# Kernel tuning notes

Hardware: AMD Instinct MI355X
Metric: run time of the kernel (lower is better)

## Reference

```python
import jax, jax.numpy as jnp
import numpy as np

N_HEAD = 16

def setup_inputs() -> dict:
    key = jax.random.key(0)
    k1, k2, k3, k4, k5 = jax.random.split(key, 5)
    B, T, C = 4, 2048, 1024
    s = 0.02
    x = jax.random.normal(k1, (B, T, C), dtype=jnp.float32)
    W_attn = jax.random.normal(k2, (C, 3 * C), dtype=jnp.float32) * s
    b_attn = jnp.zeros((3 * C,), dtype=jnp.float32)
    W_proj = jax.random.normal(k3, (C, C), dtype=jnp.float32) * s
    b_proj = jnp.zeros((C,), dtype=jnp.float32)
    return {"x": x, "W_attn": W_attn, "b_attn": b_attn, "W_proj": W_proj, "b_proj": b_proj}

def reference(x, W_attn, b_attn, W_proj, b_proj):
    B, T, C = x.shape
    H = N_HEAD
    hd = C // H
    qkv = x @ W_attn + b_attn                       # [B,T,3C]
    q, k, v = jnp.split(qkv, 3, axis=-1)            # each [B,T,C]
    # [B,H,T,hd]
    q = q.reshape(B, T, H, hd).transpose(0, 2, 1, 3)
    k = k.reshape(B, T, H, hd).transpose(0, 2, 1, 3)
    v = v.reshape(B, T, H, hd).transpose(0, 2, 1, 3)
    att = jnp.einsum('bhqd,bhkd->bhqk', q, k) * (1.0 / jnp.sqrt(jnp.float32(hd)))
    causal = jnp.tril(jnp.ones((T, T), dtype=bool))
    att = jnp.where(causal[None, None], att, jnp.float32(-jnp.inf))
    att = jax.nn.softmax(att, axis=-1)
    y = jnp.einsum('bhqk,bhkd->bhqd', att, v)       # [B,H,T,hd]
    y = y.transpose(0, 2, 1, 3).reshape(B, T, C)
    return y @ W_proj + b_proj
```

## Files before the change

### kernel.cpp

```cpp
#include <hip/hip_runtime.h>
#include <hip/hip_bf16.h>

typedef __bf16 bf16x8 __attribute__((ext_vector_type(8)));
typedef float f32x4 __attribute__((ext_vector_type(4)));

static __device__ __forceinline__ unsigned short f32_to_bf16(float f) {
    union { float f; unsigned u; } v; v.f = f;
    unsigned u = v.u;
    u += 0x7FFFu + ((u >> 16) & 1u);
    return (unsigned short)(u >> 16);
}
static __device__ __forceinline__ unsigned pack_bf16x2(float a, float b) {
    return ((unsigned)f32_to_bf16(a)) | (((unsigned)f32_to_bf16(b)) << 16);
}

static __device__ __forceinline__ void async_load16(const unsigned short* g,
                                                    unsigned short* l) {
    __builtin_amdgcn_global_load_lds(
        (__attribute__((address_space(1))) const unsigned int*)(const void*)g,
        (__attribute__((address_space(3))) unsigned int*)(void*)l,
        16, 0, 0);
}

__global__ void cast_f32_bf16(const float* __restrict__ src,
                              unsigned short* __restrict__ dst, int n4) {
    int i = blockIdx.x * blockDim.x + threadIdx.x;
    if (i < n4) {
        float4 f = ((const float4*)src)[i];
        ushort4 o;
        o.x = f32_to_bf16(f.x); o.y = f32_to_bf16(f.y);
        o.z = f32_to_bf16(f.z); o.w = f32_to_bf16(f.w);
        ((ushort4*)dst)[i] = o;
    }
}

__global__ void transpose_cast(const float* __restrict__ src,
                               unsigned short* __restrict__ dst, int R, int C) {
    __shared__ float tile[32][33];
    int c0 = blockIdx.x * 32, r0 = blockIdx.y * 32;
    int tx = threadIdx.x, ty = threadIdx.y;
    #pragma unroll
    for (int i = 0; i < 32; i += 8)
        tile[ty + i][tx] = src[(long)(r0 + ty + i) * C + c0 + tx];
    __syncthreads();
    #pragma unroll
    for (int i = 0; i < 32; i += 8)
        dst[(long)(c0 + ty + i) * R + r0 + tx] = f32_to_bf16(tile[tx][ty + i]);
}

template<bool OUT_BF16>
__global__ __launch_bounds__(256) void gemm_bt_bias(
    const unsigned short* __restrict__ A,
    const unsigned short* __restrict__ Bt,
    const float* __restrict__ bias,
    void* __restrict__ Cout,
    int M, int N, int K, int scale_ncols, float scale)
{
    __shared__ __align__(16) unsigned short As[128 * 64];
    __shared__ __align__(16) unsigned short Bs[128 * 64];

    const int tid  = threadIdx.x;
    const int m0   = blockIdx.x * 128;
    const int n0   = blockIdx.y * 128;
    const int w    = tid >> 6, lane = tid & 63;
    const int quad = lane >> 4, lr = lane & 15;
    const int wm   = (w >> 1) * 64, wn = (w & 1) * 64;

    f32x4 acc[4][4];
    #pragma unroll
    for (int i = 0; i < 4; i++)
        #pragma unroll
        for (int j = 0; j < 4; j++)
            acc[i][j] = (f32x4){0.f, 0.f, 0.f, 0.f};

    const int srow8 = lane >> 3;
    const int skoff = (lane & 7) * 8;

    for (int k0 = 0; k0 < K; k0 += 64) {
        __syncthreads();
        #pragma unroll
        for (int c = 0; c < 4; c++) {
            const int rbase = c * 32 + w * 8;
            async_load16(&A [(long)(m0 + rbase + srow8) * K + k0 + skoff], &As[rbase * 64]);
            async_load16(&Bt[(long)(n0 + rbase + srow8) * K + k0 + skoff], &Bs[rbase * 64]);
        }
        __syncthreads();

        #pragma unroll
        for (int ks = 0; ks < 2; ks++) {
            bf16x8 af[4], bfr[4];
            #pragma unroll
            for (int i = 0; i < 4; i++)
                af[i] = *(const bf16x8*)&As[(wm + i * 16 + lr) * 64 + ks * 32 + quad * 8];
            #pragma unroll
            for (int j = 0; j < 4; j++)
                bfr[j] = *(const bf16x8*)&Bs[(wn + j * 16 + lr) * 64 + ks * 32 + quad * 8];
            #pragma unroll
            for (int i = 0; i < 4; i++)
                #pragma unroll
                for (int j = 0; j < 4; j++)
                    acc[i][j] = __builtin_amdgcn_mfma_f32_16x16x32_bf16(af[i], bfr[j], acc[i][j], 0, 0, 0);
        }
    }

    #pragma unroll
    for (int i = 0; i < 4; i++) {
        #pragma unroll
        for (int j = 0; j < 4; j++) {
            int gcol = n0 + wn + j * 16 + lr;
            float bv = bias[gcol];
            float sc = (gcol < scale_ncols) ? scale : 1.0f;
            #pragma unroll
            for (int r = 0; r < 4; r++) {
                int grow = m0 + wm + i * 16 + quad * 4 + r;
                float v = (acc[i][j][r] + bv) * sc;
                if (OUT_BF16)
                    ((unsigned short*)Cout)[(long)grow * N + gcol] = f32_to_bf16(v);
                else
                    ((float*)Cout)[(long)grow * N + gcol] = v;
            }
        }
    }
}

__global__ __launch_bounds__(256) void transpose_v(
    const unsigned short* __restrict__ qkv,
    unsigned short* __restrict__ vT,
    int T, int C3, int C, int H)
{
    __shared__ __align__(16) unsigned short tile[64 * 72];
    const int tid = threadIdx.x;
    const int t0 = blockIdx.x * 64, h = blockIdx.y, b = blockIdx.z;
    const long ibase = ((long)b * T + t0) * C3 + 2 * C + h * 64;
    #pragma unroll
    for (int c = tid; c < 512; c += 256) {
        int r = c >> 3, off = (c & 7) * 8;
        *(uint4*)&tile[r * 72 + off] = *(const uint4*)&qkv[ibase + (long)r * C3 + off];
    }
    __syncthreads();
    const long obase = (long)((b * H + h) * 64) * T + t0;
    #pragma unroll
    for (int c = tid; c < 512; c += 256) {
        int d = c & 63, tc = c >> 6;
        unsigned short tmp[8];
        #pragma unroll
        for (int j = 0; j < 8; j++)
            tmp[j] = tile[(tc * 8 + j) * 72 + d];
        *(uint4*)&vT[obase + (long)d * T + tc * 8] = *(const uint4*)tmp;
    }
}

__global__ __launch_bounds__(256, 3) void attn_mfma(
    const unsigned short* __restrict__ qkv,
    const unsigned short* __restrict__ vT,
    unsigned short* __restrict__ yb,
    int T, int C3, int C, int H, int NT)
{
    constexpr int SQ = 72;
    __shared__ __align__(16) unsigned short Ks[64 * SQ];
    __shared__ __align__(16) unsigned short Vs[64 * SQ];
    __shared__ __align__(16) unsigned short Ps[128 * SQ];

    const int tid = threadIdx.x;
    const int h   = blockIdx.y;
    const int b   = blockIdx.z;
    const long rowbase = (long)b * T;
    const long vtbase  = (long)((b * H + h) * 64) * T;

    const int w = tid >> 6, lane = tid & 63;
    const int quad = lane >> 4, lr = lane & 15;

    const int r0 = tid >> 3, off0 = (tid & 7) * 8;
    const int r1 = r0 + 32;

    for (int t = 0; t < 2; t++) {
        const int qt = (t == 0) ? blockIdx.x : (NT - 1 - blockIdx.x);
        const int q0 = qt * 128;
        const int nb = 2 * qt + 2;

        const int wrow0 = w * 32;
        const int wrowmax = q0 + wrow0 + 31;

        bf16x8 aq[2][2];
        #pragma unroll
        for (int st = 0; st < 2; st++)
            #pragma unroll
            for (int ks = 0; ks < 2; ks++)
                aq[st][ks] = *(const bf16x8*)&qkv[
                    (rowbase + q0 + wrow0 + st * 16 + lr) * (long)C3 + h * 64 + ks * 32 + quad * 8];

        uint4 pk0, pk1, pv0, pv1;
        {
            long g0 = (rowbase + r0) * (long)C3 + C + h * 64 + off0;
            long g1 = (rowbase + r1) * (long)C3 + C + h * 64 + off0;
            pk0 = *(const uint4*)&qkv[g0];
            pk1 = *(const uint4*)&qkv[g1];
            pv0 = *(const uint4*)&vT[vtbase + (long)r0 * T + off0];
            pv1 = *(const uint4*)&vT[vtbase + (long)r1 * T + off0];
        }

        f32x4 oA[2][4];
        float lp[2] = {0.f, 0.f};
        #pragma unroll
        for (int st = 0; st < 2; st++)
            #pragma unroll
            for (int j = 0; j < 4; j++) oA[st][j] = (f32x4){0.f, 0.f, 0.f, 0.f};

        for (int kb = 0; kb < nb; kb++) {
            __syncthreads();
            *(uint4*)&Ks[r0 * SQ + off0] = pk0;
            *(uint4*)&Ks[r1 * SQ + off0] = pk1;
            *(uint4*)&Vs[r0 * SQ + off0] = pv0;
            *(uint4*)&Vs[r1 * SQ + off0] = pv1;
            __syncthreads();

            if (kb + 1 < nb) {
                long g0 = (rowbase + (kb + 1) * 64 + r0) * (long)C3 + C + h * 64 + off0;
                long g1 = (rowbase + (kb + 1) * 64 + r1) * (long)C3 + C + h * 64 + off0;
                pk0 = *(const uint4*)&qkv[g0];
                pk1 = *(const uint4*)&qkv[g1];
                pv0 = *(const uint4*)&vT[vtbase + (long)r0 * T + (kb + 1) * 64 + off0];
                pv1 = *(const uint4*)&vT[vtbase + (long)r1 * T + (kb + 1) * 64 + off0];
            }

            if (kb * 64 > wrowmax) continue;

            f32x4 sT[2][4];
            #pragma unroll
            for (int st = 0; st < 2; st++)
                #pragma unroll
                for (int j = 0; j < 4; j++) sT[st][j] = (f32x4){0.f, 0.f, 0.f, 0.f};
            #pragma unroll
            for (int ks = 0; ks < 2; ks++) {
                #pragma unroll
                for (int jt = 0; jt < 4; jt++) {
                    bf16x8 kf = *(const bf16x8*)&Ks[(jt * 16 + lr) * SQ + ks * 32 + quad * 8];
                    sT[0][jt] = __builtin_amdgcn_mfma_f32_16x16x32_bf16(kf, aq[0][ks], sT[0][jt], 0, 0, 0);
                    sT[1][jt] = __builtin_amdgcn_mfma_f32_16x16x32_bf16(kf, aq[1][ks], sT[1][jt], 0, 0, 0);
                }
            }

            const bool diag = (kb * 64 + 63 > q0 + wrow0);
            #pragma unroll
            for (int st = 0; st < 2; st++) {
                const int qg = q0 + wrow0 + st * 16 + lr;
                float rowsum = 0.f;
                #pragma unroll
                for (int jt = 0; jt < 4; jt++) {
                    float p[4];
                    #pragma unroll
                    for (int r = 0; r < 4; r++) {
                        float sv = sT[st][jt][r];
                        if (diag && (kb * 64 + jt * 16 + quad * 4 + r) > qg) sv = -1e30f;
                        p[r] = __builtin_amdgcn_exp2f(sv);
                        rowsum += p[r];
                    }
                    *(uint2*)&Ps[(wrow0 + st * 16 + lr) * SQ + jt * 16 + quad * 4] =
                        make_uint2(pack_bf16x2(p[0], p[1]), pack_bf16x2(p[2], p[3]));
                }
                lp[st] += rowsum;
            }

            #pragma unroll
            for (int ks = 0; ks < 2; ks++) {
                bf16x8 ap0 = *(const bf16x8*)&Ps[(wrow0 + lr) * SQ + ks * 32 + quad * 8];
                bf16x8 ap1 = *(const bf16x8*)&Ps[(wrow0 + 16 + lr) * SQ + ks * 32 + quad * 8];
                #pragma unroll
                for (int jt = 0; jt < 4; jt++) {
                    bf16x8 bv = *(const bf16x8*)&Vs[(jt * 16 + lr) * SQ + ks * 32 + quad * 8];
                    oA[0][jt] = __builtin_amdgcn_mfma_f32_16x16x32_bf16(ap0, bv, oA[0][jt], 0, 0, 0);
                    oA[1][jt] = __builtin_amdgcn_mfma_f32_16x16x32_bf16(ap1, bv, oA[1][jt], 0, 0, 0);
                }
            }
        }

        #pragma unroll
        for (int st = 0; st < 2; st++) {
            float l = lp[st];
            l += __shfl_xor(l, 16);
            l += __shfl_xor(l, 32);
            float inv = 1.f / l;
            #pragma unroll
            for (int r = 0; r < 4; r++) {
                float invr = __shfl(inv, quad * 4 + r, 16);
                long grow = rowbase + q0 + wrow0 + st * 16 + quad * 4 + r;
                #pragma unroll
                for (int jt = 0; jt < 4; jt++)
                    yb[grow * C + h * 64 + jt * 16 + lr] = f32_to_bf16(oA[st][jt][r] * invr);
            }
        }
    }
}

extern "C" void kernel_launch(void* const* d_in, const int* in_sizes, int n_in,
                              void* d_out, int out_size, void* d_ws, size_t ws_size,
                              hipStream_t stream) {
    const float* x      = (const float*)d_in[0];
    const float* W_attn = (const float*)d_in[1];
    const float* b_attn = (const float*)d_in[2];
    const float* W_proj = (const float*)d_in[3];
    const float* b_proj = (const float*)d_in[4];
    float* out = (float*)d_out;

    const int B = 4, T = 2048, C = 1024, H = 16;
    const int M  = B * T;
    const int C3 = 3 * C;
    const int NT = T / 128;
    const float scale2 = 0.18033688011112042f;

    char* ws = (char*)d_ws;
    size_t off = 0;
    auto carve = [&](size_t bytes) {
        char* p = ws + off;
        off += (bytes + 255) & ~(size_t)255;
        return p;
    };
    unsigned short* xb   = (unsigned short*)carve((size_t)M * C * 2);
    unsigned short* wat  = (unsigned short*)carve((size_t)C3 * C * 2);
    unsigned short* wpt  = (unsigned short*)carve((size_t)C * C * 2);
    unsigned short* qkvb = (unsigned short*)carve((size_t)M * C3 * 2);
    unsigned short* ybuf = (unsigned short*)carve((size_t)M * C * 2);
    unsigned short* vTb  = xb;

    cast_f32_bf16<<<(M * C / 4 + 255) / 256, 256, 0, stream>>>(x, xb, M * C / 4);
    transpose_cast<<<dim3(C3 / 32, C / 32), dim3(32, 8), 0, stream>>>(W_attn, wat, C, C3);
    transpose_cast<<<dim3(C / 32, C / 32), dim3(32, 8), 0, stream>>>(W_proj, wpt, C, C);

    gemm_bt_bias<true><<<dim3(M / 128, C3 / 128), 256, 0, stream>>>(
        xb, wat, b_attn, qkvb, M, C3, C, C, scale2);

    transpose_v<<<dim3(T / 64, H, B), 256, 0, stream>>>(qkvb, vTb, T, C3, C, H);

    attn_mfma<<<dim3(NT / 2, H, B), 256, 0, stream>>>(qkvb, vTb, ybuf, T, C3, C, H, NT);

    gemm_bt_bias<false><<<dim3(M / 128, C / 128), 256, 0, stream>>>(
        ybuf, wpt, b_proj, out, M, C, C, 0, 1.0f);
}
```

Baseline: 291.4 us.

## Fuse V transpose into QKV GEMM epilogue and XOR-swizzle GEMM LDS tiles

The QKV GEMM epilogue now writes V columns directly in the transposed [B,H,hd,T] layout into a dedicated workspace buffer when space allows. This removes the separate transpose_v kernel launch and its round trip through global memory. The GEMM's LDS tile layout also gets an XOR swizzle on the 16-byte chunk index, applied to both the async global-to-LDS loads and the MFMA fragment reads, to reduce bank conflicts. The cost is extra workspace memory, plus a branchy epilogue whose transposed stores are only 8 bytes wide and scattered.

```diff
diff --git a/kernel.cpp b/kernel.cpp
--- a/kernel.cpp
+++ b/kernel.cpp
@@ -54,7 +54,8 @@
     const unsigned short* __restrict__ Bt,
     const float* __restrict__ bias,
     void* __restrict__ Cout,
-    int M, int N, int K, int scale_ncols, float scale)
+    int M, int N, int K, int scale_ncols, float scale,
+    unsigned short* __restrict__ vT_out, int v_col0, int Tlog2, int Hn)
 {
     __shared__ __align__(16) unsigned short As[128 * 64];
     __shared__ __align__(16) unsigned short Bs[128 * 64];
@@ -74,7 +75,7 @@
             acc[i][j] = (f32x4){0.f, 0.f, 0.f, 0.f};
 
     const int srow8 = lane >> 3;
-    const int skoff = (lane & 7) * 8;
+    const int skoff = ((lane & 7) ^ srow8) * 8;
 
     for (int k0 = 0; k0 < K; k0 += 64) {
         __syncthreads();
@@ -91,10 +92,12 @@
             bf16x8 af[4], bfr[4];
             #pragma unroll
             for (int i = 0; i < 4; i++)
-                af[i] = *(const bf16x8*)&As[(wm + i * 16 + lr) * 64 + ks * 32 + quad * 8];
+                af[i] = *(const bf16x8*)&As[(wm + i * 16 + lr) * 64 +
+                                            (((ks * 4 + quad) ^ (lr & 7)) << 3)];
             #pragma unroll
             for (int j = 0; j < 4; j++)
-                bfr[j] = *(const bf16x8*)&Bs[(wn + j * 16 + lr) * 64 + ks * 32 + quad * 8];
+                bfr[j] = *(const bf16x8*)&Bs[(wn + j * 16 + lr) * 64 +
+                                             (((ks * 4 + quad) ^ (lr & 7)) << 3)];
             #pragma unroll
             for (int i = 0; i < 4; i++)
                 #pragma unroll
@@ -109,15 +112,28 @@
         for (int j = 0; j < 4; j++) {
             int gcol = n0 + wn + j * 16 + lr;
             float bv = bias[gcol];
-            float sc = (gcol < scale_ncols) ? scale : 1.0f;
-            #pragma unroll
-            for (int r = 0; r < 4; r++) {
-                int grow = m0 + wm + i * 16 + quad * 4 + r;
-                float v = (acc[i][j][r] + bv) * sc;
-                if (OUT_BF16)
-                    ((unsigned short*)Cout)[(long)grow * N + gcol] = f32_to_bf16(v);
-                else
-                    ((float*)Cout)[(long)grow * N + gcol] = v;
+            if (OUT_BF16 && vT_out != nullptr && gcol >= v_col0) {
+                int hd  = gcol - v_col0;
+                int t0g = m0 + wm + i * 16 + quad * 4;
+                int bi  = t0g >> Tlog2;
+                int tl  = t0g & ((1 << Tlog2) - 1);
+                unsigned short pk[4];
+                #pragma unroll
+                for (int r = 0; r < 4; r++)
+                    pk[r] = f32_to_bf16(acc[i][j][r] + bv);
+                *(uint2*)&vT_out[((long)bi * Hn * 64 + hd) * (1 << Tlog2) + tl] =
+                    *(const uint2*)pk;
+            } else {
+                float sc = (gcol < scale_ncols) ? scale : 1.0f;
+                #pragma unroll
+                for (int r = 0; r < 4; r++) {
+                    int grow = m0 + wm + i * 16 + quad * 4 + r;
+                    float v = (acc[i][j][r] + bv) * sc;
+                    if (OUT_BF16)
+                        ((unsigned short*)Cout)[(long)grow * N + gcol] = f32_to_bf16(v);
+                    else
+                        ((float*)Cout)[(long)grow * N + gcol] = v;
+                }
             }
         }
     }
@@ -306,6 +322,7 @@
     const int M  = B * T;
     const int C3 = 3 * C;
     const int NT = T / 128;
+    const int Tlog2 = 11;
     const float scale2 = 0.18033688011112042f;
 
     char* ws = (char*)d_ws;
@@ -320,19 +337,24 @@
     unsigned short* wpt  = (unsigned short*)carve((size_t)C * C * 2);
     unsigned short* qkvb = (unsigned short*)carve((size_t)M * C3 * 2);
     unsigned short* ybuf = (unsigned short*)carve((size_t)M * C * 2);
-    unsigned short* vTb  = xb;
+
+    const size_t vT_bytes = (size_t)B * H * 64 * T * 2;
+    bool fuse_v = (off + vT_bytes) <= ws_size;
+    unsigned short* vTb = fuse_v ? (unsigned short*)carve(vT_bytes) : xb;
 
     cast_f32_bf16<<<(M * C / 4 + 255) / 256, 256, 0, stream>>>(x, xb, M * C / 4);
     transpose_cast<<<dim3(C3 / 32, C / 32), dim3(32, 8), 0, stream>>>(W_attn, wat, C, C3);
     transpose_cast<<<dim3(C / 32, C / 32), dim3(32, 8), 0, stream>>>(W_proj, wpt, C, C);
 
     gemm_bt_bias<true><<<dim3(M / 128, C3 / 128), 256, 0, stream>>>(
-        xb, wat, b_attn, qkvb, M, C3, C, C, scale2);
-
-    transpose_v<<<dim3(T / 64, H, B), 256, 0, stream>>>(qkvb, vTb, T, C3, C, H);
+        xb, wat, b_attn, qkvb, M, C3, C, C, scale2,
+        fuse_v ? vTb : nullptr, 2 * C, Tlog2, H);
+
+    if (!fuse_v)
+        transpose_v<<<dim3(T / 64, H, B), 256, 0, stream>>>(qkvb, vTb, T, C3, C, H);
 
     attn_mfma<<<dim3(NT / 2, H, B), 256, 0, stream>>>(qkvb, vTb, ybuf, T, C3, C, H, NT);
 
     gemm_bt_bias<false><<<dim3(M / 128, C / 128), 256, 0, stream>>>(
-        ybuf, wpt, b_proj, out, M, C, C, 0, 1.0f);
-}
+        ybuf, wpt, b_proj, out, M, C, C, 0, 1.0f, nullptr, 1 << 30, Tlog2, H);
+}
```

Result: faster. 258.7 us (-11.2%).
